# Kernel tuning notes

Hardware: AMD Instinct MI355X
Metric: run time of the kernel (lower is better)

The kernel has to match this reference:

```python
import jax, jax.numpy as jnp
import numpy as np

N_NODES = 50000
N_EDGES = 600000
D_IN = 128
D_HID = 128
D_OUT = 64


def _graph_conv(x, src, dst, W, b, n):
    """DGL GraphConv, norm='both': out = D_in^{-1/2} A D_out^{-1/2} x W + b,
    degrees clamped to min 1. Weight applied before aggregation (equivalent,
    and what DGL does when in_feats >= out_feats)."""
    ones = jnp.ones(src.shape[0], x.dtype)
    deg_out = jnp.clip(jax.ops.segment_sum(ones, src, num_segments=n), 1.0)
    deg_in = jnp.clip(jax.ops.segment_sum(ones, dst, num_segments=n), 1.0)
    h = (x * jax.lax.rsqrt(deg_out)[:, None]) @ W          # [n, d_out]
    agg = jax.ops.segment_sum(h[src], dst, num_segments=n)  # SpMM: gather + scatter-add
    return agg * jax.lax.rsqrt(deg_in)[:, None] + b


def setup_inputs() -> dict:
    key = jax.random.key(0)
    ks = jax.random.split(key, 9)
    features = jax.random.normal(ks[0], (N_NODES, D_IN), jnp.float32)
    src1 = jax.random.randint(ks[1], (N_EDGES,), 0, N_NODES, jnp.int32)
    dst1 = jax.random.randint(ks[2], (N_EDGES,), 0, N_NODES, jnp.int32)
    src2 = jax.random.randint(ks[3], (N_EDGES,), 0, N_NODES, jnp.int32)
    dst2 = jax.random.randint(ks[4], (N_EDGES,), 0, N_NODES, jnp.int32)
    order_attn = jax.random.uniform(ks[5], (2,), jnp.float32)
    W1 = jax.random.normal(ks[6], (D_IN, D_HID), jnp.float32) * 0.05
    b1 = jnp.zeros((D_HID,), jnp.float32)
    W2 = jax.random.normal(ks[7], (D_HID, D_OUT), jnp.float32) * 0.05
    b2 = jnp.zeros((D_OUT,), jnp.float32)
    return {"features": features, "src1": src1, "dst1": dst1,
            "src2": src2, "dst2": dst2, "order_attn": order_attn,
            "W1": W1, "b1": b1, "W2": W2, "b2": b2}


def reference(features, src1, dst1, src2, dst2, order_attn, W1, b1, W2, b2):
    n = features.shape[0]
    # layer 1 on both graphs + weighted order-attention combine
    x11 = _graph_conv(features, src1, dst1, W1, b1, n)
    x12 = _graph_conv(features, src2, dst2, W1, b1, n)
    x1 = order_attn[0] * x11 + order_attn[1] * x12
    # layer 2 on both graphs + weighted combine
    x21 = _graph_conv(x1, src1, dst1, W2, b2, n)
    x22 = _graph_conv(x1, src2, dst2, W2, b2, n)
    return order_attn[0] * x21 + order_attn[1] * x22
```

## Files before the change

kernel.cpp:

```cpp
#include <hip/hip_runtime.h>

#define DINF 128
#define DHID 128
#define DOUTF 64

#define CHUNK 12544
#define NCHUNK 4
#define ECH 16

typedef unsigned short ushort_t;
typedef unsigned int uint_t;
typedef __attribute__((ext_vector_type(8))) short bf16x8;
typedef __attribute__((ext_vector_type(4))) float f32x4;

__device__ __forceinline__ ushort_t f2b(float x) {
    uint_t u = __float_as_uint(x);
    u += 0x7fffu + ((u >> 16) & 1u);
    return (ushort_t)(u >> 16);
}
__device__ __forceinline__ float b2f_lo(uint_t u) { return __uint_as_float(u << 16); }
__device__ __forceinline__ float b2f_hi(uint_t u) { return __uint_as_float(u & 0xffff0000u); }

__global__ void deg_priv_kernel(const int* __restrict__ s1, const int* __restrict__ d1,
                                const int* __restrict__ s2, const int* __restrict__ d2,
                                int* __restrict__ deg, int N, int ne) {
    extern __shared__ int h[];
    int t = threadIdx.x;
    for (int j = t; j < CHUNK; j += 1024) h[j] = 0;
    __syncthreads();

    const int* p = blockIdx.z == 0 ? s1 : blockIdx.z == 1 ? d1 : blockIdx.z == 2 ? s2 : d2;
    int lo = blockIdx.y * CHUNK;
    int per = (ne + ECH - 1) / ECH;
    int e0 = blockIdx.x * per;
    int e1 = e0 + per < ne ? e0 + per : ne;
    for (int i = e0 + t; i < e1; i += 1024) {
        int idx = p[i] - lo;
        if ((unsigned)idx < (unsigned)CHUNK) atomicAdd(&h[idx], 1);
    }
    __syncthreads();

    int* dz = deg + (size_t)blockIdx.z * N;
    for (int j = t; j < CHUNK; j += 1024) {
        int node = lo + j;
        int v = h[j];
        if (v && node < N) atomicAdd(&dz[node], v);
    }
}

__global__ void scan1_kernel(const int* __restrict__ d1i, const int* __restrict__ d2i,
                             int* __restrict__ offs, int* __restrict__ bsum, int n) {
    __shared__ int warp_sums[4];
    int t = threadIdx.x;
    int lane = t & 63;
    int wid = t >> 6;
    int base = blockIdx.x * 1024 + t * 4;

    int v[4];
    int tot = 0;
    #pragma unroll
    for (int j = 0; j < 4; ++j) {
        int i = base + j;
        int d = (i < n) ? d1i[i] + d2i[i] : 0;
        v[j] = d; tot += d;
    }
    int x = tot;
    #pragma unroll
    for (int off = 1; off < 64; off <<= 1) {
        int y = __shfl_up(x, off, 64);
        if (lane >= off) x += y;
    }
    if (lane == 63) warp_sums[wid] = x;
    __syncthreads();
    int wbase = 0;
    for (int w = 0; w < wid; ++w) wbase += warp_sums[w];
    int run = wbase + x - tot;
    #pragma unroll
    for (int j = 0; j < 4; ++j) {
        int i = base + j;
        if (i < n) offs[i] = run;
        run += v[j];
    }
    if (t == 255) bsum[blockIdx.x] = run;
}

__global__ void scan2_kernel(int* __restrict__ bsum, int* __restrict__ offs, int nb, int n) {
    int lane = threadIdx.x;
    int run = 0;
    for (int base = 0; base < nb; base += 64) {
        int i = base + lane;
        int v = (i < nb) ? bsum[i] : 0;
        int x = v;
        #pragma unroll
        for (int off = 1; off < 64; off <<= 1) {
            int y = __shfl_up(x, off, 64);
            if (lane >= off) x += y;
        }
        if (i < nb) bsum[i] = run + x - v;
        run += __shfl(x, 63, 64);
    }
    if (lane == 0) offs[n] = run;
}

__global__ void scan3_kernel(int* __restrict__ offs, int* __restrict__ cursor,
                             const int* __restrict__ bsum, int n) {
    int base = blockIdx.x * 1024 + threadIdx.x * 4;
    int add = bsum[blockIdx.x];
    #pragma unroll
    for (int j = 0; j < 4; ++j) {
        int i = base + j;
        if (i < n) { int o = offs[i] + add; offs[i] = o; cursor[i] = o; }
    }
}

__global__ void fill2_kernel(const int* __restrict__ src1, const int* __restrict__ dst1,
                             const int* __restrict__ src2, const int* __restrict__ dst2,
                             const int* __restrict__ deg, const float* __restrict__ attn,
                             int* __restrict__ cursor, int2* __restrict__ csr, int N, int ne) {
    int i = blockIdx.x * 256 + threadIdx.x;
    if (i >= ne) return;
    int g = blockIdx.y;
    const int* src = g == 0 ? src1 : src2;
    const int* dst = g == 0 ? dst1 : dst2;
    const int* deg_out = deg + (size_t)(2 * g) * N;
    const int* deg_in  = deg + (size_t)(2 * g + 1) * N;
    int s = src[i];
    int d = dst[i];
    int pos = atomicAdd(&cursor[d], 1);
    float w = attn[g] * rsqrtf(fmaxf((float)deg_in[d], 1.0f))
                      * rsqrtf(fmaxf((float)deg_out[s], 1.0f));
    csr[pos] = make_int2(s, __float_as_int(w));
}

__global__ void wconv2_kernel(const float* __restrict__ W1, const float* __restrict__ W2,
                              ushort_t* __restrict__ Wt1, ushort_t* __restrict__ Wt2) {
    int tid = blockIdx.x * 256 + threadIdx.x;
    if (tid < 128 * 128) {
        int ncol = tid / 128, k = tid % 128;
        Wt1[tid] = f2b(W1[(size_t)k * 128 + ncol]);
    } else if (tid < 128 * 128 + 64 * 128) {
        int t2 = tid - 128 * 128;
        int ncol = t2 / 128, k = t2 % 128;
        Wt2[t2] = f2b(W2[(size_t)k * 64 + ncol]);
    }
}

template<int NOUT, bool F32IN>
__global__ __launch_bounds__(256) void mfma_gemm_kernel(const void* __restrict__ Xv,
                                                        const ushort_t* __restrict__ Wt,
                                                        ushort_t* __restrict__ Y, int n) {
    constexpr int CT = NOUT / 16;
    const int lane = threadIdx.x & 63;
    const int wv = threadIdx.x >> 6;
    const int row0 = blockIdx.x * 64 + wv * 16;
    const int arow = row0 + (lane & 15);
    const int arc = arow < n ? arow : (n - 1);

    f32x4 acc[CT];
    #pragma unroll
    for (int ct = 0; ct < CT; ++ct) acc[ct] = (f32x4)(0.f);

    #pragma unroll
    for (int kk = 0; kk < 4; ++kk) {
        const int k0 = kk * 32 + (lane >> 4) * 8;
        bf16x8 a;
        if (F32IN) {
            const float* xp = (const float*)Xv + (size_t)arc * 128 + k0;
            float4 u0 = *(const float4*)xp;
            float4 u1 = *(const float4*)(xp + 4);
            a[0] = (short)f2b(u0.x); a[1] = (short)f2b(u0.y);
            a[2] = (short)f2b(u0.z); a[3] = (short)f2b(u0.w);
            a[4] = (short)f2b(u1.x); a[5] = (short)f2b(u1.y);
            a[6] = (short)f2b(u1.z); a[7] = (short)f2b(u1.w);
        } else {
            a = *(const bf16x8*)((const ushort_t*)Xv + (size_t)arc * 128 + k0);
        }
        #pragma unroll
        for (int ct = 0; ct < CT; ++ct) {
            bf16x8 b = *(const bf16x8*)(Wt + (size_t)(ct * 16 + (lane & 15)) * 128 + k0);
            acc[ct] = __builtin_amdgcn_mfma_f32_16x16x32_bf16(a, b, acc[ct], 0, 0, 0);
        }
    }

    const int orow0 = row0 + (lane >> 4) * 4;
    const int col = lane & 15;
    #pragma unroll
    for (int ct = 0; ct < CT; ++ct) {
        #pragma unroll
        for (int r = 0; r < 4; ++r) {
            int row = orow0 + r;
            if (row < n) Y[(size_t)row * NOUT + ct * 16 + col] = f2b(acc[ct][r]);
        }
    }
}

__global__ void agg128_kernel(const ushort_t* __restrict__ V, const int* __restrict__ offs,
                              const int2* __restrict__ csr, const float* __restrict__ bias,
                              const float* __restrict__ attn, uint_t* __restrict__ out, int n) {
    int wid = (int)(((size_t)blockIdx.x * blockDim.x + threadIdx.x) >> 6);
    int lane = threadIdx.x & 63;
    if (wid >= n) return;
    int e0 = offs[wid], e1 = offs[wid + 1];

    float acc0 = 0.f, acc1 = 0.f;

    int e = e0;
    for (; e + 8 <= e1; e += 8) {
        int2 cv[8];
        uint_t u[8];
        #pragma unroll
        for (int j = 0; j < 8; ++j) cv[j] = csr[e + j];
        #pragma unroll
        for (int j = 0; j < 8; ++j)
            u[j] = ((const uint_t*)(V + (size_t)cv[j].x * 128))[lane];
        #pragma unroll
        for (int j = 0; j < 8; ++j) {
            float w = __int_as_float(cv[j].y);
            acc0 += w * b2f_lo(u[j]);
            acc1 += w * b2f_hi(u[j]);
        }
    }
    if (e + 4 <= e1) {
        int2 cv[4];
        uint_t u[4];
        #pragma unroll
        for (int j = 0; j < 4; ++j) cv[j] = csr[e + j];
        #pragma unroll
        for (int j = 0; j < 4; ++j)
            u[j] = ((const uint_t*)(V + (size_t)cv[j].x * 128))[lane];
        #pragma unroll
        for (int j = 0; j < 4; ++j) {
            float w = __int_as_float(cv[j].y);
            acc0 += w * b2f_lo(u[j]);
            acc1 += w * b2f_hi(u[j]);
        }
        e += 4;
    }
    for (; e < e1; ++e) {
        int2 cv = csr[e];
        float w = __int_as_float(cv.y);
        uint_t u = ((const uint_t*)(V + (size_t)cv.x * 128))[lane];
        acc0 += w * b2f_lo(u); acc1 += w * b2f_hi(u);
    }

    float bs = attn[0] + attn[1];
    float2 bb = ((const float2*)bias)[lane];
    float o0 = acc0 + bs * bb.x;
    float o1 = acc1 + bs * bb.y;
    out[(size_t)wid * 64 + lane] = (uint_t)f2b(o0) | ((uint_t)f2b(o1) << 16);
}

__global__ void agg64_kernel(const ushort_t* __restrict__ V, const int* __restrict__ offs,
                             const int2* __restrict__ csr, const float* __restrict__ bias,
                             const float* __restrict__ attn, float* __restrict__ out, int n) {
    int wid = (int)(((size_t)blockIdx.x * blockDim.x + threadIdx.x) >> 6);
    int lane = threadIdx.x & 63;
    int half = lane >> 5;
    int hl = lane & 31;
    if (wid >= n) return;
    int e0 = offs[wid], e1 = offs[wid + 1];

    float acc0 = 0.f, acc1 = 0.f;

    int e = e0;
    for (; e + 8 <= e1; e += 8) {
        int2 cv[4];
        uint_t u[4];
        #pragma unroll
        for (int j = 0; j < 4; ++j) cv[j] = csr[e + 2 * j + half];
        #pragma unroll
        for (int j = 0; j < 4; ++j)
            u[j] = ((const uint_t*)(V + (size_t)cv[j].x * 64))[hl];
        #pragma unroll
        for (int j = 0; j < 4; ++j) {
            float w = __int_as_float(cv[j].y);
            acc0 += w * b2f_lo(u[j]);
            acc1 += w * b2f_hi(u[j]);
        }
    }
    for (; e + 2 <= e1; e += 2) {
        int2 cv = csr[e + half];
        float w = __int_as_float(cv.y);
        uint_t u = ((const uint_t*)(V + (size_t)cv.x * 64))[hl];
        acc0 += w * b2f_lo(u); acc1 += w * b2f_hi(u);
    }
    if (e < e1 && half == 0) {
        int2 cv = csr[e];
        float w = __int_as_float(cv.y);
        uint_t u = ((const uint_t*)(V + (size_t)cv.x * 64))[hl];
        acc0 += w * b2f_lo(u); acc1 += w * b2f_hi(u);
    }

    acc0 += __shfl_xor(acc0, 32, 64);
    acc1 += __shfl_xor(acc1, 32, 64);

    if (half == 0) {
        float bs = attn[0] + attn[1];
        float2 bb = ((const float2*)bias)[hl];
        float2 o = make_float2(acc0 + bs * bb.x, acc1 + bs * bb.y);
        ((float2*)(out + (size_t)wid * 64))[hl] = o;
    }
}

extern "C" void kernel_launch(void* const* d_in, const int* in_sizes, int n_in,
                              void* d_out, int out_size, void* d_ws, size_t ws_size,
                              hipStream_t stream) {
    const float* feat = (const float*)d_in[0];
    const int* src1   = (const int*)d_in[1];
    const int* dst1   = (const int*)d_in[2];
    const int* src2   = (const int*)d_in[3];
    const int* dst2   = (const int*)d_in[4];
    const float* attn = (const float*)d_in[5];
    const float* W1   = (const float*)d_in[6];
    const float* b1   = (const float*)d_in[7];
    const float* W2   = (const float*)d_in[8];
    const float* b2   = (const float*)d_in[9];
    float* out = (float*)d_out;

    const int N  = in_sizes[0] / DINF;
    const int NE = in_sizes[1];
    const int NB = (N + 1023) / 1024;

    ushort_t* Wt1 = (ushort_t*)d_ws;
    ushort_t* Wt2 = Wt1 + 128 * 128;
    ushort_t* A   = Wt2 + 64 * 128;
    ushort_t* B   = A + (size_t)N * DHID;
    ushort_t* C   = B + (size_t)N * DHID;
    int2* csr   = (int2*)(C + (size_t)N * DOUTF);
    int* offs   = (int*)(csr + 2 * (size_t)NE);
    int* cursor = offs + (N + 1);
    int* deg    = cursor + N;
    int* d1i = deg + N;
    int* d2i = deg + 3 * (size_t)N;
    int* bsum = deg + 4 * (size_t)N;

    hipMemsetAsync(deg, 0, sizeof(int) * 4 * (size_t)N, stream);

    wconv2_kernel<<<(128 * 128 + 64 * 128 + 255) / 256, 256, 0, stream>>>(W1, W2, Wt1, Wt2);

    deg_priv_kernel<<<dim3(ECH, NCHUNK, 4), 1024, CHUNK * sizeof(int), stream>>>(
        src1, dst1, src2, dst2, deg, N, NE);

    scan1_kernel<<<NB, 256, 0, stream>>>(d1i, d2i, offs, bsum, N);
    scan2_kernel<<<1, 64, 0, stream>>>(bsum, offs, NB, N);
    scan3_kernel<<<NB, 256, 0, stream>>>(offs, cursor, bsum, N);

    int eb = (NE + 255) / 256;
    fill2_kernel<<<dim3(eb, 2), 256, 0, stream>>>(src1, dst1, src2, dst2, deg, attn,
                                                  cursor, csr, N, NE);

    int gb = (N + 63) / 64;
    mfma_gemm_kernel<DHID, true><<<gb, 256, 0, stream>>>(feat, Wt1, A, N);
    agg128_kernel<<<(N + 3) / 4, 256, 0, stream>>>(A, offs, csr, b1, attn, (uint_t*)B, N);

    mfma_gemm_kernel<DOUTF, false><<<gb, 256, 0, stream>>>(B, Wt2, C, N);
    agg64_kernel<<<(N + 3) / 4, 256, 0, stream>>>(C, offs, csr, b2, attn, out, N);
}
```

Measured before the change: 212.9 us.

## Split CSR fill cursors into eight groups to cut atomic contention, stage edges

Builds the CSR as eight independent sub-CSRs keyed by edge-block group, using a new histogram kernel and a scan over 8*N segments. The fill kernel's cursor atomics are spread across eight counters per node instead of one. The aggregation kernels merge the eight segment ranges per node, staging up to CAP edges into shared memory before gathering and falling back to global reads for overflow. This adds an extra histogram pass, a larger scan, and segment-merge overhead in the aggregation kernels.

```diff
diff --git a/kernel.cpp b/kernel.cpp
--- a/kernel.cpp
+++ b/kernel.cpp
@@ -7,6 +7,9 @@
 #define CHUNK 12544
 #define NCHUNK 4
 #define ECH 16
+#define ESL 4
+#define NGRP 8
+#define CAP 96
 
 typedef unsigned short ushort_t;
 typedef unsigned int uint_t;
@@ -48,8 +51,45 @@
     }
 }
 
-__global__ void scan1_kernel(const int* __restrict__ d1i, const int* __restrict__ d2i,
-                             int* __restrict__ offs, int* __restrict__ bsum, int n) {
+__global__ void cnt_hist_kernel(const int* __restrict__ dst1, const int* __restrict__ dst2,
+                                int* __restrict__ cnt, int N, int ne, int eb) {
+    extern __shared__ int h[];
+    int t = threadIdx.x;
+    for (int j = t; j < CHUNK; j += 1024) h[j] = 0;
+    __syncthreads();
+
+    int lo = blockIdx.x * CHUNK;
+    int g = blockIdx.y;
+    int q = blockIdx.z;
+
+    for (int graph = 0; graph < 2; ++graph) {
+        const int* dst = graph ? dst2 : dst1;
+        int base = graph * eb;
+        int r0 = (g - base) & 7;
+        if (r0 >= eb) continue;
+        int K = (eb - r0 + 7) / 8;
+        int k0 = (int)(((long long)K * q) / ESL);
+        int k1 = (int)(((long long)K * (q + 1)) / ESL);
+        for (int idx = k0 * 256 + t; idx < k1 * 256; idx += 1024) {
+            int r = r0 + 8 * (idx >> 8);
+            int i = r * 256 + (idx & 255);
+            if (i < ne) {
+                int d = dst[i] - lo;
+                if ((unsigned)d < (unsigned)CHUNK) atomicAdd(&h[d], 1);
+            }
+        }
+    }
+    __syncthreads();
+
+    int* cq = cnt + (size_t)q * (8 * (size_t)N) + (size_t)g * N;
+    for (int j = t; j < CHUNK; j += 1024) {
+        int node = lo + j;
+        if (node < N) cq[node] = h[j];
+    }
+}
+
+__global__ void scan1_kernel(const int* __restrict__ cnt, int* __restrict__ offs,
+                             int* __restrict__ bsum, int m) {
     __shared__ int warp_sums[4];
     int t = threadIdx.x;
     int lane = t & 63;
@@ -61,7 +101,8 @@
     #pragma unroll
     for (int j = 0; j < 4; ++j) {
         int i = base + j;
-        int d = (i < n) ? d1i[i] + d2i[i] : 0;
+        int d = 0;
+        if (i < m) d = cnt[i] + cnt[m + i] + cnt[2 * (size_t)m + i] + cnt[3 * (size_t)m + i];
         v[j] = d; tot += d;
     }
     int x = tot;
@@ -78,13 +119,13 @@
     #pragma unroll
     for (int j = 0; j < 4; ++j) {
         int i = base + j;
-        if (i < n) offs[i] = run;
+        if (i < m) offs[i] = run;
         run += v[j];
     }
     if (t == 255) bsum[blockIdx.x] = run;
 }
 
-__global__ void scan2_kernel(int* __restrict__ bsum, int* __restrict__ offs, int nb, int n) {
+__global__ void scan2_kernel(int* __restrict__ bsum, int* __restrict__ offs, int nb, int m) {
     int lane = threadIdx.x;
     int run = 0;
     for (int base = 0; base < nb; base += 64) {
@@ -99,36 +140,39 @@
         if (i < nb) bsum[i] = run + x - v;
         run += __shfl(x, 63, 64);
     }
-    if (lane == 0) offs[n] = run;
+    if (lane == 0) offs[m] = run;
 }
 
 __global__ void scan3_kernel(int* __restrict__ offs, int* __restrict__ cursor,
-                             const int* __restrict__ bsum, int n) {
+                             const int* __restrict__ bsum, int m) {
     int base = blockIdx.x * 1024 + threadIdx.x * 4;
     int add = bsum[blockIdx.x];
     #pragma unroll
     for (int j = 0; j < 4; ++j) {
         int i = base + j;
-        if (i < n) { int o = offs[i] + add; offs[i] = o; cursor[i] = o; }
+        if (i < m) { int o = offs[i] + add; offs[i] = o; cursor[i] = o; }
     }
 }
 
 __global__ void fill2_kernel(const int* __restrict__ src1, const int* __restrict__ dst1,
                              const int* __restrict__ src2, const int* __restrict__ dst2,
                              const int* __restrict__ deg, const float* __restrict__ attn,
-                             int* __restrict__ cursor, int2* __restrict__ csr, int N, int ne) {
-    int i = blockIdx.x * 256 + threadIdx.x;
+                             int* __restrict__ cursor, int2* __restrict__ csr,
+                             int N, int ne, int eb) {
+    int b = blockIdx.x;
+    int i = b * 256 + threadIdx.x;
     if (i >= ne) return;
-    int g = blockIdx.y;
-    const int* src = g == 0 ? src1 : src2;
-    const int* dst = g == 0 ? dst1 : dst2;
-    const int* deg_out = deg + (size_t)(2 * g) * N;
-    const int* deg_in  = deg + (size_t)(2 * g + 1) * N;
+    int gr = blockIdx.y;
+    int g = ((gr ? eb : 0) + b) & 7;
+    const int* src = gr == 0 ? src1 : src2;
+    const int* dst = gr == 0 ? dst1 : dst2;
+    const int* deg_out = deg + (size_t)(2 * gr) * N;
+    const int* deg_in  = deg + (size_t)(2 * gr + 1) * N;
     int s = src[i];
     int d = dst[i];
-    int pos = atomicAdd(&cursor[d], 1);
-    float w = attn[g] * rsqrtf(fmaxf((float)deg_in[d], 1.0f))
-                      * rsqrtf(fmaxf((float)deg_out[s], 1.0f));
+    int pos = atomicAdd(&cursor[(size_t)g * N + d], 1);
+    float w = attn[gr] * rsqrtf(fmaxf((float)deg_in[d], 1.0f))
+                       * rsqrtf(fmaxf((float)deg_out[s], 1.0f));
     csr[pos] = make_int2(s, __float_as_int(w));
 }
 
@@ -194,107 +238,172 @@
     }
 }
 
+__device__ __forceinline__ int stage_edges(const int* __restrict__ offs,
+                                           const int2* __restrict__ csr,
+                                           int2* __restrict__ el,
+                                           int n, int wid, int lane, bool valid,
+                                           int c0[8], int c1[8], int eg[8]) {
+    int myE0 = 0, myLen = 0;
+    if (valid && lane < 8) {
+        myE0 = offs[(size_t)lane * n + wid];
+        myLen = offs[(size_t)lane * n + wid + 1] - myE0;
+    }
+    int inc = myLen;
+    #pragma unroll
+    for (int off = 1; off < 8; off <<= 1) {
+        int y = __shfl_up(inc, off, 8);
+        if ((lane & 7) >= off) inc += y;
+    }
+    int exc = inc - myLen;
+    int total = __shfl(inc, 7, 64);
+    #pragma unroll
+    for (int g = 0; g < 8; ++g) {
+        c0[g] = __shfl(exc, g, 64);
+        c1[g] = __shfl(inc, g, 64);
+        eg[g] = __shfl(myE0, g, 64);
+    }
+    int tot = total < CAP ? total : CAP;
+    for (int k = lane; k < tot; k += 64) {
+        int ea = 0;
+        #pragma unroll
+        for (int g = 0; g < 8; ++g)
+            if (k >= c0[g] && k < c1[g]) ea = eg[g] + (k - c0[g]);
+        el[k] = csr[ea];
+    }
+    return total;
+}
+
 __global__ void agg128_kernel(const ushort_t* __restrict__ V, const int* __restrict__ offs,
                               const int2* __restrict__ csr, const float* __restrict__ bias,
                               const float* __restrict__ attn, uint_t* __restrict__ out, int n) {
-    int wid = (int)(((size_t)blockIdx.x * blockDim.x + threadIdx.x) >> 6);
+    __shared__ int2 el[4][CAP];
+    int wv = threadIdx.x >> 6;
     int lane = threadIdx.x & 63;
-    if (wid >= n) return;
-    int e0 = offs[wid], e1 = offs[wid + 1];
+    int wid = blockIdx.x * 4 + wv;
+    bool valid = wid < n;
+
+    int c0[8], c1[8], eg[8];
+    int total = stage_edges(offs, csr, el[wv], n, valid ? wid : 0, lane, valid, c0, c1, eg);
+    __syncthreads();
+    int tot = total < CAP ? total : CAP;
 
     float acc0 = 0.f, acc1 = 0.f;
-
-    int e = e0;
-    for (; e + 8 <= e1; e += 8) {
-        int2 cv[8];
-        uint_t u[8];
-        #pragma unroll
-        for (int j = 0; j < 8; ++j) cv[j] = csr[e + j];
+    int e = 0;
+    for (; e + 8 <= tot; e += 8) {
+        int2 cv[8]; uint_t u[8];
+        #pragma unroll
+        for (int j = 0; j < 8; ++j) cv[j] = el[wv][e + j];
         #pragma unroll
         for (int j = 0; j < 8; ++j)
             u[j] = ((const uint_t*)(V + (size_t)cv[j].x * 128))[lane];
         #pragma unroll
         for (int j = 0; j < 8; ++j) {
             float w = __int_as_float(cv[j].y);
-            acc0 += w * b2f_lo(u[j]);
-            acc1 += w * b2f_hi(u[j]);
-        }
-    }
-    if (e + 4 <= e1) {
-        int2 cv[4];
-        uint_t u[4];
-        #pragma unroll
-        for (int j = 0; j < 4; ++j) cv[j] = csr[e + j];
+            acc0 += w * b2f_lo(u[j]); acc1 += w * b2f_hi(u[j]);
+        }
+    }
+    if (e + 4 <= tot) {
+        int2 cv[4]; uint_t u[4];
+        #pragma unroll
+        for (int j = 0; j < 4; ++j) cv[j] = el[wv][e + j];
         #pragma unroll
         for (int j = 0; j < 4; ++j)
             u[j] = ((const uint_t*)(V + (size_t)cv[j].x * 128))[lane];
         #pragma unroll
         for (int j = 0; j < 4; ++j) {
             float w = __int_as_float(cv[j].y);
-            acc0 += w * b2f_lo(u[j]);
-            acc1 += w * b2f_hi(u[j]);
+            acc0 += w * b2f_lo(u[j]); acc1 += w * b2f_hi(u[j]);
         }
         e += 4;
     }
-    for (; e < e1; ++e) {
-        int2 cv = csr[e];
+    for (; e < tot; ++e) {
+        int2 cv = el[wv][e];
         float w = __int_as_float(cv.y);
         uint_t u = ((const uint_t*)(V + (size_t)cv.x * 128))[lane];
         acc0 += w * b2f_lo(u); acc1 += w * b2f_hi(u);
     }
-
-    float bs = attn[0] + attn[1];
-    float2 bb = ((const float2*)bias)[lane];
-    float o0 = acc0 + bs * bb.x;
-    float o1 = acc1 + bs * bb.y;
-    out[(size_t)wid * 64 + lane] = (uint_t)f2b(o0) | ((uint_t)f2b(o1) << 16);
+    if (total > CAP) {
+        #pragma unroll
+        for (int g = 0; g < 8; ++g) {
+            int s0 = c0[g] > CAP ? c0[g] : CAP;
+            for (int k = s0; k < c1[g]; ++k) {
+                int2 cv = csr[eg[g] + (k - c0[g])];
+                float w = __int_as_float(cv.y);
+                uint_t u = ((const uint_t*)(V + (size_t)cv.x * 128))[lane];
+                acc0 += w * b2f_lo(u); acc1 += w * b2f_hi(u);
+            }
+        }
+    }
+
+    if (valid) {
+        float bs = attn[0] + attn[1];
+        float2 bb = ((const float2*)bias)[lane];
+        float o0 = acc0 + bs * bb.x;
+        float o1 = acc1 + bs * bb.y;
+        out[(size_t)wid * 64 + lane] = (uint_t)f2b(o0) | ((uint_t)f2b(o1) << 16);
+    }
 }
 
 __global__ void agg64_kernel(const ushort_t* __restrict__ V, const int* __restrict__ offs,
                              const int2* __restrict__ csr, const float* __restrict__ bias,
                              const float* __restrict__ attn, float* __restrict__ out, int n) {
-    int wid = (int)(((size_t)blockIdx.x * blockDim.x + threadIdx.x) >> 6);
+    __shared__ int2 el[4][CAP];
+    int wv = threadIdx.x >> 6;
     int lane = threadIdx.x & 63;
     int half = lane >> 5;
     int hl = lane & 31;
-    if (wid >= n) return;
-    int e0 = offs[wid], e1 = offs[wid + 1];
+    int wid = blockIdx.x * 4 + wv;
+    bool valid = wid < n;
+
+    int c0[8], c1[8], eg[8];
+    int total = stage_edges(offs, csr, el[wv], n, valid ? wid : 0, lane, valid, c0, c1, eg);
+    __syncthreads();
+    int tot = total < CAP ? total : CAP;
 
     float acc0 = 0.f, acc1 = 0.f;
-
-    int e = e0;
-    for (; e + 8 <= e1; e += 8) {
-        int2 cv[4];
-        uint_t u[4];
-        #pragma unroll
-        for (int j = 0; j < 4; ++j) cv[j] = csr[e + 2 * j + half];
+    int e = 0;
+    for (; e + 8 <= tot; e += 8) {
+        int2 cv[4]; uint_t u[4];
+        #pragma unroll
+        for (int j = 0; j < 4; ++j) cv[j] = el[wv][e + 2 * j + half];
         #pragma unroll
         for (int j = 0; j < 4; ++j)
             u[j] = ((const uint_t*)(V + (size_t)cv[j].x * 64))[hl];
         #pragma unroll
         for (int j = 0; j < 4; ++j) {
             float w = __int_as_float(cv[j].y);
-            acc0 += w * b2f_lo(u[j]);
-            acc1 += w * b2f_hi(u[j]);
-        }
-    }
-    for (; e + 2 <= e1; e += 2) {
-        int2 cv = csr[e + half];
+            acc0 += w * b2f_lo(u[j]); acc1 += w * b2f_hi(u[j]);
+        }
+    }
+    for (; e + 2 <= tot; e += 2) {
+        int2 cv = el[wv][e + half];
         float w = __int_as_float(cv.y);
         uint_t u = ((const uint_t*)(V + (size_t)cv.x * 64))[hl];
         acc0 += w * b2f_lo(u); acc1 += w * b2f_hi(u);
     }
-    if (e < e1 && half == 0) {
-        int2 cv = csr[e];
+    if (e < tot && half == 0) {
+        int2 cv = el[wv][e];
         float w = __int_as_float(cv.y);
         uint_t u = ((const uint_t*)(V + (size_t)cv.x * 64))[hl];
         acc0 += w * b2f_lo(u); acc1 += w * b2f_hi(u);
     }
+    if (total > CAP && half == 0) {
+        #pragma unroll
+        for (int g = 0; g < 8; ++g) {
+            int s0 = c0[g] > CAP ? c0[g] : CAP;
+            for (int k = s0; k < c1[g]; ++k) {
+                int2 cv = csr[eg[g] + (k - c0[g])];
+                float w = __int_as_float(cv.y);
+                uint_t u = ((const uint_t*)(V + (size_t)cv.x * 64))[hl];
+                acc0 += w * b2f_lo(u); acc1 += w * b2f_hi(u);
+            }
+        }
+    }
 
     acc0 += __shfl_xor(acc0, 32, 64);
     acc1 += __shfl_xor(acc1, 32, 64);
 
-    if (half == 0) {
+    if (valid && half == 0) {
         float bs = attn[0] + attn[1];
         float2 bb = ((const float2*)bias)[hl];
         float2 o = make_float2(acc0 + bs * bb.x, acc1 + bs * bb.y);
@@ -319,7 +428,9 @@
 
     const int N  = in_sizes[0] / DINF;
     const int NE = in_sizes[1];
-    const int NB = (N + 1023) / 1024;
+    const int eb = (NE + 255) / 256;
+    const int M  = NGRP * N;
+    const int NB2 = (M + 1023) / 1024;
 
     ushort_t* Wt1 = (ushort_t*)d_ws;
     ushort_t* Wt2 = Wt1 + 128 * 128;
@@ -328,11 +439,10 @@
     ushort_t* C   = B + (size_t)N * DHID;
     int2* csr   = (int2*)(C + (size_t)N * DOUTF);
     int* offs   = (int*)(csr + 2 * (size_t)NE);
-    int* cursor = offs + (N + 1);
-    int* deg    = cursor + N;
-    int* d1i = deg + N;
-    int* d2i = deg + 3 * (size_t)N;
-    int* bsum = deg + 4 * (size_t)N;
+    int* cursor = offs + (M + 1);
+    int* deg    = cursor + M;
+    int* cnt    = deg + 4 * (size_t)N;
+    int* bsum   = cnt + (size_t)ESL * M;
 
     hipMemsetAsync(deg, 0, sizeof(int) * 4 * (size_t)N, stream);
 
@@ -341,18 +451,21 @@
     deg_priv_kernel<<<dim3(ECH, NCHUNK, 4), 1024, CHUNK * sizeof(int), stream>>>(
         src1, dst1, src2, dst2, deg, N, NE);
 
-    scan1_kernel<<<NB, 256, 0, stream>>>(d1i, d2i, offs, bsum, N);
-    scan2_kernel<<<1, 64, 0, stream>>>(bsum, offs, NB, N);
-    scan3_kernel<<<NB, 256, 0, stream>>>(offs, cursor, bsum, N);
-
-    int eb = (NE + 255) / 256;
+    cnt_hist_kernel<<<dim3(NCHUNK, NGRP, ESL), 1024, CHUNK * sizeof(int), stream>>>(
+        dst1, dst2, cnt, N, NE, eb);
+
+    scan1_kernel<<<NB2, 256, 0, stream>>>(cnt, offs, bsum, M);
+    scan2_kernel<<<1, 64, 0, stream>>>(bsum, offs, NB2, M);
+    scan3_kernel<<<NB2, 256, 0, stream>>>(offs, cursor, bsum, M);
+
     fill2_kernel<<<dim3(eb, 2), 256, 0, stream>>>(src1, dst1, src2, dst2, deg, attn,
-                                                  cursor, csr, N, NE);
+                                                  cursor, csr, N, NE, eb);
 
     int gb = (N + 63) / 64;
+    int ab = (N + 3) / 4;
     mfma_gemm_kernel<DHID, true><<<gb, 256, 0, stream>>>(feat, Wt1, A, N);
-    agg128_kernel<<<(N + 3) / 4, 256, 0, stream>>>(A, offs, csr, b1, attn, (uint_t*)B, N);
+    agg128_kernel<<<ab, 256, 0, stream>>>(A, offs, csr, b1, attn, (uint_t*)B, N);
 
     mfma_gemm_kernel<DOUTF, false><<<gb, 256, 0, stream>>>(B, Wt2, C, N);
-    agg64_kernel<<<(N + 3) / 4, 256, 0, stream>>>(C, offs, csr, b2, attn, out, N);
-}
+    agg64_kernel<<<ab, 256, 0, stream>>>(C, offs, csr, b2, attn, out, N);
+}
```

Result: slower. 232.6 us (+9.3%).

## Replace global-atomic CSR build with per-slice LDS histograms and LDS cursors

Applied to the files above, without the earlier changes.

Degree counting now writes per-slice, per-node counts without global atomics, and a separate kernel reduces them into precomputed rsqrt normalizers. The CSR offsets come from a scan over the node-major (node, slice) count matrix. This lets the fill kernel place edges using shared-memory cursors per node chunk and slice, replacing global atomicAdd on a cursor array. It also drops the memset. In exchange it adds a larger scan (16x N entries), an extra reduction kernel, and fill blocks that each rescan their edge slice for every node chunk.

```diff
diff --git a/kernel.cpp b/kernel.cpp
--- a/kernel.cpp
+++ b/kernel.cpp
@@ -6,7 +6,7 @@
 
 #define CHUNK 12544
 #define NCHUNK 4
-#define ECH 16
+#define NSLICE 16
 
 typedef unsigned short ushort_t;
 typedef unsigned int uint_t;
@@ -21,48 +21,76 @@
 __device__ __forceinline__ float b2f_lo(uint_t u) { return __uint_as_float(u << 16); }
 __device__ __forceinline__ float b2f_hi(uint_t u) { return __uint_as_float(u & 0xffff0000u); }
 
-__global__ void deg_priv_kernel(const int* __restrict__ s1, const int* __restrict__ d1,
-                                const int* __restrict__ s2, const int* __restrict__ d2,
-                                int* __restrict__ deg, int N, int ne) {
+__global__ void cnt_kernel(const int* __restrict__ s1, const int* __restrict__ d1,
+                           const int* __restrict__ s2, const int* __restrict__ d2,
+                           int* __restrict__ cntS, int* __restrict__ cntD, int N, int ne) {
     extern __shared__ int h[];
     int t = threadIdx.x;
     for (int j = t; j < CHUNK; j += 1024) h[j] = 0;
     __syncthreads();
 
-    const int* p = blockIdx.z == 0 ? s1 : blockIdx.z == 1 ? d1 : blockIdx.z == 2 ? s2 : d2;
-    int lo = blockIdx.y * CHUNK;
-    int per = (ne + ECH - 1) / ECH;
-    int e0 = blockIdx.x * per;
-    int e1 = e0 + per < ne ? e0 + per : ne;
+    int lo = blockIdx.x * CHUNK;
+    int q = blockIdx.y;
+    bool isSrc = blockIdx.z == 0;
+    int SL = (2 * ne) / NSLICE;
+    int g = q >= (NSLICE / 2);
+    const int* p = g ? (isSrc ? s2 : d2) : (isSrc ? s1 : d1);
+    int base = g ? ne : 0;
+    int e0 = q * SL - base;
+    int e1 = e0 + SL;
     for (int i = e0 + t; i < e1; i += 1024) {
-        int idx = p[i] - lo;
-        if ((unsigned)idx < (unsigned)CHUNK) atomicAdd(&h[idx], 1);
+        int v = p[i] - lo;
+        if ((unsigned)v < (unsigned)CHUNK) atomicAdd(&h[v], 1);
     }
     __syncthreads();
 
-    int* dz = deg + (size_t)blockIdx.z * N;
+    int* c = (isSrc ? cntS : cntD) + (size_t)q * N;
     for (int j = t; j < CHUNK; j += 1024) {
         int node = lo + j;
-        int v = h[j];
-        if (v && node < N) atomicAdd(&dz[node], v);
-    }
-}
-
-__global__ void scan1_kernel(const int* __restrict__ d1i, const int* __restrict__ d2i,
-                             int* __restrict__ offs, int* __restrict__ bsum, int n) {
+        if (node < N) c[node] = h[j];
+    }
+}
+
+__global__ void degred_kernel(const int* __restrict__ cntS, const int* __restrict__ cntD,
+                              float* __restrict__ rs, int N) {
+    int v = blockIdx.x * 256 + threadIdx.x;
+    if (v >= N) return;
+    int o1 = 0, i1 = 0, o2 = 0, i2 = 0;
+    #pragma unroll
+    for (int q = 0; q < NSLICE / 2; ++q) {
+        o1 += cntS[(size_t)q * N + v];
+        i1 += cntD[(size_t)q * N + v];
+    }
+    #pragma unroll
+    for (int q = NSLICE / 2; q < NSLICE; ++q) {
+        o2 += cntS[(size_t)q * N + v];
+        i2 += cntD[(size_t)q * N + v];
+    }
+    rs[v]                  = rsqrtf(fmaxf((float)o1, 1.0f));
+    rs[N + v]              = rsqrtf(fmaxf((float)i1, 1.0f));
+    rs[2 * (size_t)N + v]  = rsqrtf(fmaxf((float)o2, 1.0f));
+    rs[3 * (size_t)N + v]  = rsqrtf(fmaxf((float)i2, 1.0f));
+}
+
+__global__ void scan1_kernel(const int* __restrict__ cntD, int* __restrict__ offs,
+                             int* __restrict__ bsum, int N, int m) {
     __shared__ int warp_sums[4];
     int t = threadIdx.x;
     int lane = t & 63;
     int wid = t >> 6;
     int base = blockIdx.x * 1024 + t * 4;
 
-    int v[4];
+    int v4[4];
     int tot = 0;
     #pragma unroll
     for (int j = 0; j < 4; ++j) {
         int i = base + j;
-        int d = (i < n) ? d1i[i] + d2i[i] : 0;
-        v[j] = d; tot += d;
+        int d = 0;
+        if (i < m) {
+            int v = i >> 4, q = i & 15;
+            d = cntD[(size_t)q * N + v];
+        }
+        v4[j] = d; tot += d;
     }
     int x = tot;
     #pragma unroll
@@ -78,13 +106,13 @@
     #pragma unroll
     for (int j = 0; j < 4; ++j) {
         int i = base + j;
-        if (i < n) offs[i] = run;
-        run += v[j];
+        if (i < m) offs[i] = run;
+        run += v4[j];
     }
     if (t == 255) bsum[blockIdx.x] = run;
 }
 
-__global__ void scan2_kernel(int* __restrict__ bsum, int* __restrict__ offs, int nb, int n) {
+__global__ void scan2_kernel(int* __restrict__ bsum, int* __restrict__ offs, int nb, int m) {
     int lane = threadIdx.x;
     int run = 0;
     for (int base = 0; base < nb; base += 64) {
@@ -99,37 +127,52 @@
         if (i < nb) bsum[i] = run + x - v;
         run += __shfl(x, 63, 64);
     }
-    if (lane == 0) offs[n] = run;
-}
-
-__global__ void scan3_kernel(int* __restrict__ offs, int* __restrict__ cursor,
-                             const int* __restrict__ bsum, int n) {
+    if (lane == 0) offs[m] = run;
+}
+
+__global__ void scan3_kernel(int* __restrict__ offs, const int* __restrict__ bsum, int m) {
     int base = blockIdx.x * 1024 + threadIdx.x * 4;
     int add = bsum[blockIdx.x];
     #pragma unroll
     for (int j = 0; j < 4; ++j) {
         int i = base + j;
-        if (i < n) { int o = offs[i] + add; offs[i] = o; cursor[i] = o; }
-    }
-}
-
-__global__ void fill2_kernel(const int* __restrict__ src1, const int* __restrict__ dst1,
-                             const int* __restrict__ src2, const int* __restrict__ dst2,
-                             const int* __restrict__ deg, const float* __restrict__ attn,
-                             int* __restrict__ cursor, int2* __restrict__ csr, int N, int ne) {
-    int i = blockIdx.x * 256 + threadIdx.x;
-    if (i >= ne) return;
-    int g = blockIdx.y;
-    const int* src = g == 0 ? src1 : src2;
-    const int* dst = g == 0 ? dst1 : dst2;
-    const int* deg_out = deg + (size_t)(2 * g) * N;
-    const int* deg_in  = deg + (size_t)(2 * g + 1) * N;
-    int s = src[i];
-    int d = dst[i];
-    int pos = atomicAdd(&cursor[d], 1);
-    float w = attn[g] * rsqrtf(fmaxf((float)deg_in[d], 1.0f))
-                      * rsqrtf(fmaxf((float)deg_out[s], 1.0f));
-    csr[pos] = make_int2(s, __float_as_int(w));
+        if (i < m) offs[i] += add;
+    }
+}
+
+__global__ void fill_kernel(const int* __restrict__ s1, const int* __restrict__ d1,
+                            const int* __restrict__ s2, const int* __restrict__ d2,
+                            const float* __restrict__ rs, const float* __restrict__ attn,
+                            const int* __restrict__ offs, int2* __restrict__ csr,
+                            int N, int ne) {
+    extern __shared__ int cur[];
+    int t = threadIdx.x;
+    int lo = blockIdx.x * CHUNK;
+    int q = blockIdx.y;
+    int lim = N - lo < CHUNK ? N - lo : CHUNK;
+    for (int j = t; j < lim; j += 1024)
+        cur[j] = offs[(size_t)(lo + j) * NSLICE + q];
+    __syncthreads();
+
+    int SL = (2 * ne) / NSLICE;
+    int g = q >= (NSLICE / 2);
+    const int* src = g ? s2 : s1;
+    const int* dst = g ? d2 : d1;
+    const float* rs_o = rs + (size_t)(2 * g) * N;
+    const float* rs_i = rs + (size_t)(2 * g + 1) * N;
+    float ag = attn[g];
+    int base = g ? ne : 0;
+    int e0 = q * SL - base;
+    int e1 = e0 + SL;
+    for (int i = e0 + t; i < e1; i += 1024) {
+        int d = dst[i] - lo;
+        if ((unsigned)d < (unsigned)lim) {
+            int s = src[i];
+            int pos = atomicAdd(&cur[d], 1);
+            float w = ag * rs_i[lo + d] * rs_o[s];
+            csr[pos] = make_int2(s, __float_as_int(w));
+        }
+    }
 }
 
 __global__ void wconv2_kernel(const float* __restrict__ W1, const float* __restrict__ W2,
@@ -200,14 +243,13 @@
     int wid = (int)(((size_t)blockIdx.x * blockDim.x + threadIdx.x) >> 6);
     int lane = threadIdx.x & 63;
     if (wid >= n) return;
-    int e0 = offs[wid], e1 = offs[wid + 1];
+    int e0 = offs[(size_t)wid << 4];
+    int e1 = offs[((size_t)wid << 4) + 16];
 
     float acc0 = 0.f, acc1 = 0.f;
-
     int e = e0;
     for (; e + 8 <= e1; e += 8) {
-        int2 cv[8];
-        uint_t u[8];
+        int2 cv[8]; uint_t u[8];
         #pragma unroll
         for (int j = 0; j < 8; ++j) cv[j] = csr[e + j];
         #pragma unroll
@@ -216,13 +258,11 @@
         #pragma unroll
         for (int j = 0; j < 8; ++j) {
             float w = __int_as_float(cv[j].y);
-            acc0 += w * b2f_lo(u[j]);
-            acc1 += w * b2f_hi(u[j]);
+            acc0 += w * b2f_lo(u[j]); acc1 += w * b2f_hi(u[j]);
         }
     }
     if (e + 4 <= e1) {
-        int2 cv[4];
-        uint_t u[4];
+        int2 cv[4]; uint_t u[4];
         #pragma unroll
         for (int j = 0; j < 4; ++j) cv[j] = csr[e + j];
         #pragma unroll
@@ -231,8 +271,7 @@
         #pragma unroll
         for (int j = 0; j < 4; ++j) {
             float w = __int_as_float(cv[j].y);
-            acc0 += w * b2f_lo(u[j]);
-            acc1 += w * b2f_hi(u[j]);
+            acc0 += w * b2f_lo(u[j]); acc1 += w * b2f_hi(u[j]);
         }
         e += 4;
     }
@@ -258,14 +297,13 @@
     int half = lane >> 5;
     int hl = lane & 31;
     if (wid >= n) return;
-    int e0 = offs[wid], e1 = offs[wid + 1];
+    int e0 = offs[(size_t)wid << 4];
+    int e1 = offs[((size_t)wid << 4) + 16];
 
     float acc0 = 0.f, acc1 = 0.f;
-
     int e = e0;
     for (; e + 8 <= e1; e += 8) {
-        int2 cv[4];
-        uint_t u[4];
+        int2 cv[4]; uint_t u[4];
         #pragma unroll
         for (int j = 0; j < 4; ++j) cv[j] = csr[e + 2 * j + half];
         #pragma unroll
@@ -274,8 +312,7 @@
         #pragma unroll
         for (int j = 0; j < 4; ++j) {
             float w = __int_as_float(cv[j].y);
-            acc0 += w * b2f_lo(u[j]);
-            acc1 += w * b2f_hi(u[j]);
+            acc0 += w * b2f_lo(u[j]); acc1 += w * b2f_hi(u[j]);
         }
     }
     for (; e + 2 <= e1; e += 2) {
@@ -319,7 +356,8 @@
 
     const int N  = in_sizes[0] / DINF;
     const int NE = in_sizes[1];
-    const int NB = (N + 1023) / 1024;
+    const int M  = NSLICE * N;
+    const int NB2 = (M + 1023) / 1024;
 
     ushort_t* Wt1 = (ushort_t*)d_ws;
     ushort_t* Wt2 = Wt1 + 128 * 128;
@@ -328,31 +366,30 @@
     ushort_t* C   = B + (size_t)N * DHID;
     int2* csr   = (int2*)(C + (size_t)N * DOUTF);
     int* offs   = (int*)(csr + 2 * (size_t)NE);
-    int* cursor = offs + (N + 1);
-    int* deg    = cursor + N;
-    int* d1i = deg + N;
-    int* d2i = deg + 3 * (size_t)N;
-    int* bsum = deg + 4 * (size_t)N;
-
-    hipMemsetAsync(deg, 0, sizeof(int) * 4 * (size_t)N, stream);
+    int* cntS   = offs + (M + 1);
+    int* cntD   = cntS + M;
+    float* rs   = (float*)(cntD + M);
+    int* bsum   = (int*)(rs + 4 * (size_t)N);
 
     wconv2_kernel<<<(128 * 128 + 64 * 128 + 255) / 256, 256, 0, stream>>>(W1, W2, Wt1, Wt2);
 
-    deg_priv_kernel<<<dim3(ECH, NCHUNK, 4), 1024, CHUNK * sizeof(int), stream>>>(
-        src1, dst1, src2, dst2, deg, N, NE);
-
-    scan1_kernel<<<NB, 256, 0, stream>>>(d1i, d2i, offs, bsum, N);
-    scan2_kernel<<<1, 64, 0, stream>>>(bsum, offs, NB, N);
-    scan3_kernel<<<NB, 256, 0, stream>>>(offs, cursor, bsum, N);
-
-    int eb = (NE + 255) / 256;
-    fill2_kernel<<<dim3(eb, 2), 256, 0, stream>>>(src1, dst1, src2, dst2, deg, attn,
-                                                  cursor, csr, N, NE);
+    cnt_kernel<<<dim3(NCHUNK, NSLICE, 2), 1024, CHUNK * sizeof(int), stream>>>(
+        src1, dst1, src2, dst2, cntS, cntD, N, NE);
+
+    degred_kernel<<<(N + 255) / 256, 256, 0, stream>>>(cntS, cntD, rs, N);
+
+    scan1_kernel<<<NB2, 256, 0, stream>>>(cntD, offs, bsum, N, M);
+    scan2_kernel<<<1, 64, 0, stream>>>(bsum, offs, NB2, M);
+    scan3_kernel<<<NB2, 256, 0, stream>>>(offs, bsum, M);
+
+    fill_kernel<<<dim3(NCHUNK, NSLICE), 1024, CHUNK * sizeof(int), stream>>>(
+        src1, dst1, src2, dst2, rs, attn, offs, csr, N, NE);
 
     int gb = (N + 63) / 64;
+    int ab = (N + 3) / 4;
     mfma_gemm_kernel<DHID, true><<<gb, 256, 0, stream>>>(feat, Wt1, A, N);
-    agg128_kernel<<<(N + 3) / 4, 256, 0, stream>>>(A, offs, csr, b1, attn, (uint_t*)B, N);
+    agg128_kernel<<<ab, 256, 0, stream>>>(A, offs, csr, b1, attn, (uint_t*)B, N);
 
     mfma_gemm_kernel<DOUTF, false><<<gb, 256, 0, stream>>>(B, Wt2, C, N);
-    agg64_kernel<<<(N + 3) / 4, 256, 0, stream>>>(C, offs, csr, b2, attn, out, N);
-}
+    agg64_kernel<<<ab, 256, 0, stream>>>(C, offs, csr, b2, attn, out, N);
+}
```

After: 244.8 us. +15.0%, slower.
